# Kernel optimization log

Hardware: AMD Instinct MI355X
Metric: run time of the kernel (lower is better)

Reference implementation:

```python
import jax, jax.numpy as jnp
import numpy as np

B, S, W = 32, 128, 16
E, CD, H, P = 256, 64, 512, 256
V, CV, NC = 50000, 256, 6
CK, WK = 8, 64  # merged char/word conv kernel sizes


def conv1d(x, w, b):
    # x: [N, Cin, L], w: [Cout, Cin, K] -> [N, Cout, L-K+1] (VALID)
    y = jax.lax.conv_general_dilated(x, w, (1,), 'VALID',
                                     dimension_numbers=('NCH', 'OIH', 'NCH'))
    return y + b[None, :, None]


def setup_inputs() -> dict:
    key = jax.random.key(0)
    ks = iter(jax.random.split(key, 40))
    nrm = lambda shape: jax.random.normal(next(ks), shape, dtype=jnp.float32) * 0.05
    return {
        'seq': jax.random.randint(next(ks), (B, S), 0, V),
        'seq_char': jax.random.randint(next(ks), (B, S, W), 0, CV),
        'classes': jnp.arange(NC, dtype=jnp.int32).reshape(NC, 1),
        'embed_w': nrm((V, E)),
        'char_embed_w': nrm((CV, CD)),
        'class_embed_w': nrm((NC, E)),
        'char_conv_w': nrm((CD, CD, CK)), 'char_conv_b': nrm((CD,)),
        'word_conv_w': nrm((E, E + CD, WK)), 'word_conv_b': nrm((E,)),
        'f_Wih': nrm((4 * H, E + CD)), 'f_Whh': nrm((4 * H, H)), 'f_b': nrm((4 * H,)),
        'b_Wih': nrm((4 * H, E + CD)), 'b_Whh': nrm((4 * H, H)), 'b_b': nrm((4 * H,)),
        'attend': nrm((E, 2 * H)),
        'd_Wih': nrm((6 * H, E + 2 * H)), 'd_Whh': nrm((6 * H, 2 * H)),
        'd_bih': nrm((6 * H,)), 'd_bhh': nrm((6 * H,)),
        'proj_w': nrm((P, 2 * H)), 'proj_b': nrm((P,)),
        'cls_w': nrm((2, P)), 'cls_b': nrm((2,)),
    }


def reference(seq, seq_char, classes, embed_w, char_embed_w, class_embed_w,
              char_conv_w, char_conv_b, word_conv_w, word_conv_b,
              f_Wih, f_Whh, f_b, b_Wih, b_Whh, b_b, attend,
              d_Wih, d_Whh, d_bih, d_bhh, proj_w, proj_b, cls_w, cls_b):
    # eval-mode forward (dropout p=0.01 is identity at eval time)
    Bq, Sq = seq.shape
    pad_mask = (seq > 0).astype(jnp.float32)            # [B,S]
    word_e = jnp.tanh(embed_w[seq])                     # [B,S,E]
    # char CNN: all char convs share kernel size -> merged into one conv
    ce = char_embed_w[seq_char]                         # [B,S,W,CD]
    ce = ce.reshape(Bq * Sq, W, CD).transpose(0, 2, 1)  # [B*S, CD, W]
    char_feat = jnp.tanh(conv1d(ce, char_conv_w, char_conv_b).mean(-1).reshape(Bq, Sq, CD))
    x = jnp.concatenate([word_e, char_feat], -1)        # [B,S,E+CD]
    # word CNN over full sequence -> [B,E]
    conv_seq = jnp.tanh(conv1d(x.transpose(0, 2, 1), word_conv_w, word_conv_b).mean(-1))
    # BiLSTM; backward direction uses seq_emb[-i], i.e. order [0, S-1, ..., 1] (as in original)
    xs = x.transpose(1, 0, 2)                           # [S,B,E+CD]
    xs_b = xs[(-jnp.arange(Sq)) % Sq]

    def lstm_scan(Wih, Whh, b, inputs):
        def step(carry, xt):
            h, c = carry
            g = xt @ Wih.T + h @ Whh.T + b
            i, f, gg, o = jnp.split(g, 4, axis=-1)
            c = jax.nn.sigmoid(f) * c + jax.nn.sigmoid(i) * jnp.tanh(gg)
            h = jax.nn.sigmoid(o) * jnp.tanh(c)
            return (h, c), h
        h0 = jnp.zeros((Bq, H), x.dtype)
        _, hs = jax.lax.scan(step, (h0, h0), inputs)
        return hs

    fouts = lstm_scan(f_Wih, f_Whh, f_b, xs)            # [S,B,H]
    bouts = lstm_scan(b_Wih, b_Whh, b_b, xs_b)[::-1]    # reversed, as in original
    seq_repr = jnp.concatenate([fouts, bouts], -1)      # [S,B,2H]
    h0 = seq_repr[-1]                                   # decoder init state [B,2H]
    seq_repr = seq_repr.transpose(1, 0, 2)              # [B,S,2H]
    # class attention: the expanded attn rows are identical across positions,
    # so sum over dim 1 of the [B,S,S] bmm equals S * tanh(a_c) . seq_repr[b,t]
    a = jnp.tanh(jnp.tanh(class_embed_w[classes[:, 0]])) @ attend   # [C,2H]
    scores = Sq * jnp.einsum('ch,bth->cbt', jnp.tanh(a), seq_repr)  # [C,B,S]
    scores = scores * pad_mask[None]
    att_ctx = jnp.einsum('cbt,bth->cbh', jnp.tanh(scores), seq_repr)  # [C,B,2H]

    def gru_step(h, ctx):
        inp = jnp.concatenate([conv_seq, ctx], -1)      # [B, E+2H]
        gi = inp @ d_Wih.T + d_bih
        gh = h @ d_Whh.T + d_bhh
        ir, iz, inn = jnp.split(gi, 3, -1)
        hr, hz, hn = jnp.split(gh, 3, -1)
        r = jax.nn.sigmoid(ir + hr)
        z = jax.nn.sigmoid(iz + hz)
        n = jnp.tanh(inn + r * hn)
        h_new = jnp.tanh((1 - z) * n + z * h)           # post-tanh state fed back (as in original)
        logits = (h_new @ proj_w.T + proj_b) @ cls_w.T + cls_b
        return h_new, jax.nn.log_softmax(logits, -1)

    _, outs = jax.lax.scan(gru_step, h0, att_ctx)       # [C,B,2]
    return outs
```

## Files before the change

### kernel.cpp

```cpp
#include <hip/hip_runtime.h>

typedef __bf16 bf16_t;
typedef __bf16 bf16x8 __attribute__((ext_vector_type(8)));
typedef float f32x4 __attribute__((ext_vector_type(4)));

static constexpr int BB = 32, SS = 128, WW = 16, EE = 256, CDm = 64, HH = 512, PP = 256;
static constexpr int EC = 320;
static constexpr int H2 = 1024;
static constexpr int G6 = 3072;
static constexpr int NKT = 28;
static constexpr int NKTX = 12;

__device__ __forceinline__ float sigm(float x){ return 1.f/(1.f + expf(-x)); }

__global__ void k_embed(const int* __restrict__ seq, const float* __restrict__ embed_w,
                        float* __restrict__ x, float* __restrict__ mask){
  int bs = blockIdx.x; int c = threadIdx.x;
  int wid = seq[bs];
  x[(size_t)bs*EC + c] = tanhf(embed_w[(size_t)wid*EE + c]);
  if (c == 0) mask[bs] = (wid > 0) ? 1.f : 0.f;
}

__global__ void k_cbar(const int* __restrict__ seq_char, const float* __restrict__ cemb,
                       float* __restrict__ cbar){
  int bs = blockIdx.x; int c = threadIdx.x;
  float ce[WW];
  #pragma unroll
  for (int p = 0; p < WW; ++p){
    int id = seq_char[bs*WW + p];
    ce[p] = cemb[(size_t)id*CDm + c];
  }
  #pragma unroll
  for (int k = 0; k < 8; ++k){
    float s = 0.f;
    #pragma unroll
    for (int p = 0; p < 9; ++p) s += ce[k+p];
    cbar[(size_t)bs*512 + c*8 + k] = s * (1.f/9.f);
  }
}

__global__ __launch_bounds__(64) void k_xbar(const float* __restrict__ x, float* __restrict__ xbar){
  __shared__ float xl[64][129];
  int gid = blockIdx.x*64 + threadIdx.x;
  int b = gid / EC, c = gid % EC;
  int tl = threadIdx.x;
  for (int t = 0; t < SS; ++t) xl[tl][t] = x[((size_t)b*SS + t)*EC + c];
  float s = 0.f;
  for (int t = 0; t < 65; ++t) s += xl[tl][t];
  const float inv = 1.f/65.f;
  float* o = &xbar[(size_t)(b*EC + c)*64];
  o[0] = s*inv;
  for (int k = 1; k < 64; ++k){ s += xl[tl][k+64] - xl[tl][k-1]; o[k] = s*inv; }
}

template<int BM,int BN,int TM,int TN>
__global__ __launch_bounds__(256) void k_gemm(const float* __restrict__ A,
    const float* __restrict__ Wm, float* __restrict__ part,
    int M, int N, int K, int kslice){
  __shared__ float As[32][BM+4];
  __shared__ float Ws[32][BN+4];
  const int tid = threadIdx.x;
  const int tx = tid & 15, ty = tid >> 4;
  const int m0 = blockIdx.x*BM, n0 = blockIdx.y*BN, ks = blockIdx.z;
  const int kb = ks*kslice;
  float acc[TM][TN];
  #pragma unroll
  for (int i = 0; i < TM; ++i)
    #pragma unroll
    for (int j = 0; j < TN; ++j) acc[i][j] = 0.f;
  for (int kt = 0; kt < kslice; kt += 32){
    constexpr int AIT = (BM*8)/256;
    #pragma unroll
    for (int it = 0; it < AIT; ++it){
      int ch = tid + it*256;
      int r = ch >> 3, kc = (ch & 7)*4;
      float4 v = *(const float4*)(A + (size_t)(m0+r)*K + kb + kt + kc);
      As[kc+0][r]=v.x; As[kc+1][r]=v.y; As[kc+2][r]=v.z; As[kc+3][r]=v.w;
    }
    constexpr int WIT = (BN*8)/256;
    #pragma unroll
    for (int it = 0; it < WIT; ++it){
      int ch = tid + it*256;
      int r = ch >> 3, kc = (ch & 7)*4;
      float4 v = *(const float4*)(Wm + (size_t)(n0+r)*K + kb + kt + kc);
      Ws[kc+0][r]=v.x; Ws[kc+1][r]=v.y; Ws[kc+2][r]=v.z; Ws[kc+3][r]=v.w;
    }
    __syncthreads();
    #pragma unroll
    for (int kk = 0; kk < 32; ++kk){
      float a[TM], wv[TN];
      #pragma unroll
      for (int i = 0; i < TM; ++i) a[i] = As[kk][ty*TM+i];
      #pragma unroll
      for (int j = 0; j < TN; ++j) wv[j] = Ws[kk][tx*TN+j];
      #pragma unroll
      for (int i = 0; i < TM; ++i)
        #pragma unroll
        for (int j = 0; j < TN; ++j) acc[i][j] = fmaf(a[i], wv[j], acc[i][j]);
    }
    __syncthreads();
  }
  #pragma unroll
  for (int i = 0; i < TM; ++i){
    int row = m0 + ty*TM + i;
    #pragma unroll
    for (int j = 0; j < TN; ++j){
      int col = n0 + tx*TN + j;
      part[((size_t)ks*M + row)*N + col] = acc[i][j];
    }
  }
}

__global__ __launch_bounds__(64) void k_fin(const float* __restrict__ part,
    const float* __restrict__ bias, float* __restrict__ out,
    int M, int N, int KS, int ldc, int act){
  int col = blockIdx.x*64 + threadIdx.x;
  int row = blockIdx.y;
  float v = bias ? bias[col] : 0.f;
  for (int ks = 0; ks < KS; ++ks) v += part[((size_t)ks*M + row)*N + col];
  if (act) v = tanhf(v);
  out[(size_t)row*ldc + col] = v;
}

__global__ __launch_bounds__(64) void k_packw(const float* __restrict__ fWih, const float* __restrict__ fWhh,
    const float* __restrict__ bWih, const float* __restrict__ bWhh, bf16_t* __restrict__ Wp){
  int id = blockIdx.x;
  int kt = id % NKT; id /= NKT;
  int slice = id % 32; int dir = id / 32;
  int l = threadIdx.x;
  const float* Whh = dir ? bWhh : fWhh;
  const float* Wih = dir ? bWih : fWih;
  int krow = (l >> 4)*8;
  for (int nt = 0; nt < 4; ++nt){
    int row = nt*512 + slice*16 + (l & 15);
    bf16_t* dst = &Wp[((((size_t)(dir*32+slice)*NKT + kt)*4 + nt)*64 + l)*8];
    if (kt < 16){
      const float* src = &Whh[(size_t)row*512 + kt*32 + krow];
      #pragma unroll
      for (int r = 0; r < 8; ++r) dst[r] = (bf16_t)src[r];
    } else {
      int kx = (kt-16)*32 + krow;
      if (kx + 8 <= 320){
        const float* src = &Wih[(size_t)row*320 + kx];
        #pragma unroll
        for (int r = 0; r < 8; ++r) dst[r] = (bf16_t)src[r];
      } else {
        #pragma unroll
        for (int r = 0; r < 8; ++r) dst[r] = (bf16_t)0.f;
      }
    }
  }
}

__global__ __launch_bounds__(64) void k_packdw(const float* __restrict__ W, bf16_t* __restrict__ Wo){
  int id = blockIdx.x;
  int kt = id % 32; id /= 32;
  int nt = id % 3;  int wg = id / 3;
  int l = threadIdx.x;
  int col = nt*1024 + wg*16 + (l & 15);
  int k0 = kt*32 + (l >> 4)*8;
  bf16_t* dst = Wo + (((size_t)(wg*3 + nt)*32 + kt)*64 + l)*8;
  const float* src = W + (size_t)col*1024 + k0;
  #pragma unroll
  for (int r = 0; r < 8; ++r) dst[r] = (bf16_t)src[r];
}

__global__ __launch_bounds__(64) void k_packpw(const float* __restrict__ W, bf16_t* __restrict__ Wo){
  int id = blockIdx.x;
  int kt = id & 31, wg = id >> 5;
  int l = threadIdx.x;
  int col = wg*16 + (l & 15);
  int k0 = kt*32 + (l >> 4)*8;
  bf16_t* dst = Wo + (((size_t)wg*32 + kt)*64 + l)*8;
  const float* src = W + (size_t)col*1024 + k0;
  #pragma unroll
  for (int r = 0; r < 8; ++r) dst[r] = (bf16_t)src[r];
}

__global__ __launch_bounds__(64) void k_packx(const float* __restrict__ x, bf16_t* __restrict__ xp){
  int id = blockIdx.x;
  int ktx = id % NKTX; id /= NKTX;
  int mt = id & 1; int t = id >> 1;
  int l = threadIdx.x;
  int b = (l & 15) + 16*mt;
  int c = ktx*32 + (l >> 4)*8;
  bf16_t* dst = &xp[(((size_t)t*2 + mt)*NKTX + ktx)*64*8 + (size_t)l*8];
  if (c + 8 <= EC){
    const float* src = &x[((size_t)b*SS + t)*EC + c];
    #pragma unroll
    for (int r = 0; r < 8; ++r) dst[r] = (bf16_t)src[r];
  } else {
    #pragma unroll
    for (int r = 0; r < 8; ++r) dst[r] = (bf16_t)0.f;
  }
}

__global__ __launch_bounds__(256) void k_zero(unsigned int* __restrict__ base){
  int i = blockIdx.x*256 + threadIdx.x;
  if (i < 35840) __hip_atomic_store(base + i, 0u, __ATOMIC_RELAXED, __HIP_MEMORY_SCOPE_AGENT);
}

__global__ __launch_bounds__(64) void k_hprep(const float* __restrict__ seq_repr, bf16_t* __restrict__ hdp){
  int mt = blockIdx.x >> 5, kt = blockIdx.x & 31, l = threadIdx.x;
  int b = mt*16 + (l & 15);
  int jb = kt*32 + (l >> 4)*8;
  const float* src = &seq_repr[((size_t)b*SS + 127)*H2 + jb];
  unsigned* dst = (unsigned*)(hdp + (((size_t)mt*32 + kt)*64 + l)*8);
  #pragma unroll
  for (int p = 0; p < 4; ++p){
    unsigned pk = (unsigned)__builtin_bit_cast(unsigned short, (bf16_t)src[2*p])
                | ((unsigned)__builtin_bit_cast(unsigned short, (bf16_t)src[2*p+1]) << 16);
    __hip_atomic_store(dst + p, pk, __ATOMIC_RELAXED, __HIP_MEMORY_SCOPE_AGENT);
  }
}

__global__ __launch_bounds__(256, 1) void k_lstm(const bf16_t* __restrict__ Wp,
    const bf16_t* __restrict__ xp, bf16_t* __restrict__ hp,
    const float* __restrict__ fb, const float* __restrict__ bb,
    float* __restrict__ seq_repr, unsigned int* __restrict__ lf){
  const int wg = blockIdx.x;
  const int dir = wg >> 5, slice = wg & 31;
  const int tid = threadIdx.x;
  const int wv = tid >> 6, lane = tid & 63;
  __shared__ __align__(16) bf16_t Wl[NKT*4*64*8];
  __shared__ float red[4][32][65];
  __shared__ float bias_l[64];
  __shared__ float c_l[16][32];
  {
    const uint4* src = (const uint4*)(Wp + ((size_t)(dir*32 + slice))*NKT*4*64*8);
    uint4* dst = (uint4*)Wl;
    for (int i = tid; i < NKT*4*64*8/8; i += 256) dst[i] = src[i];
  }
  if (tid < 64){
    const float* bv = dir ? bb : fb;
    bias_l[tid] = bv[(tid >> 4)*512 + slice*16 + (tid & 15)];
  }
  ((float*)c_l)[tid]       = 0.f;
  ((float*)c_l)[tid + 256] = 0.f;
  __syncthreads();

  union HU { unsigned long long u[2]; bf16x8 v; };

  for (int t = 0; t < SS; ++t){
    const int ph = t & 1;
    const int s = dir ? ((SS - t) & 127) : t;
    f32x4 acc[2][4];
    f32x4 zero = {0.f,0.f,0.f,0.f};
    #pragma unroll
    for (int m = 0; m < 2; ++m)
      #pragma unroll
      for (int n = 0; n < 4; ++n) acc[m][n] = zero;

    const bf16_t* xb = xp + (size_t)s*2*NKTX*64*8;
    bf16x8 ax[3][2];
    #pragma unroll
    for (int i = 0; i < 3; ++i){
      int ktx = wv*3 + i;
      #pragma unroll
      for (int m = 0; m < 2; ++m)
        ax[i][m] = *reinterpret_cast<const bf16x8*>(xb + (((size_t)m*NKTX + ktx)*64 + lane)*8);
    }
    #pragma unroll
    for (int i = 0; i < 3; ++i){
      int kt = 16 + wv*3 + i;
      #pragma unroll
      for (int nt = 0; nt < 4; ++nt){
        bf16x8 Bf = *reinterpret_cast<const bf16x8*>(&Wl[(((size_t)kt*4 + nt)*64 + lane)*8]);
        acc[0][nt] = __builtin_amdgcn_mfma_f32_16x16x32_bf16(ax[i][0], Bf, acc[0][nt], 0, 0, 0);
        acc[1][nt] = __builtin_amdgcn_mfma_f32_16x16x32_bf16(ax[i][1], Bf, acc[1][nt], 0, 0, 0);
      }
    }
    if (t > 0 && lane < 8){
      int prod = dir*32 + (wv + 4*(lane >> 1))*2 + (lane & 1);
      const unsigned int* fp = lf + prod*16;
      unsigned tgt = (unsigned)t;
      for(;;){
        unsigned v = __hip_atomic_load(fp, __ATOMIC_RELAXED, __HIP_MEMORY_SCOPE_AGENT);
        if (__ballot(v < tgt) == 0ull) break;
      }
    }
    const bf16_t* hb_ = hp + ((size_t)(ph*2 + dir))*2*16*64*8;
    bf16x8 ah[4][2];
    #pragma unroll
    for (int i = 0; i < 4; ++i){
      int kt = wv + 4*i;
      #pragma unroll
      for (int m = 0; m < 2; ++m){
        const unsigned long long* p =
            (const unsigned long long*)(hb_ + (((size_t)m*16 + kt)*64 + lane)*8);
        HU u;
        u.u[0] = __hip_atomic_load(p,     __ATOMIC_RELAXED, __HIP_MEMORY_SCOPE_AGENT);
        u.u[1] = __hip_atomic_load(p + 1, __ATOMIC_RELAXED, __HIP_MEMORY_SCOPE_AGENT);
        ah[i][m] = u.v;
      }
    }
    #pragma unroll
    for (int i = 0; i < 4; ++i){
      int kt = wv + 4*i;
      #pragma unroll
      for (int nt = 0; nt < 4; ++nt){
        bf16x8 Bf = *reinterpret_cast<const bf16x8*>(&Wl[(((size_t)kt*4 + nt)*64 + lane)*8]);
        acc[0][nt] = __builtin_amdgcn_mfma_f32_16x16x32_bf16(ah[i][0], Bf, acc[0][nt], 0, 0, 0);
        acc[1][nt] = __builtin_amdgcn_mfma_f32_16x16x32_bf16(ah[i][1], Bf, acc[1][nt], 0, 0, 0);
      }
    }
    {
      int r0 = (lane >> 4)*4, cc = lane & 15;
      #pragma unroll
      for (int m = 0; m < 2; ++m)
        #pragma unroll
        for (int n = 0; n < 4; ++n)
          #pragma unroll
          for (int e = 0; e < 4; ++e)
            red[wv][m*16 + r0 + e][n*16 + cc] = acc[m][n][e];
    }
    __syncthreads();
    {
      int b = tid & 31, jjp = tid >> 5;
      float hv[2];
      #pragma unroll
      for (int u2 = 0; u2 < 2; ++u2){
        int jj = jjp*2 + u2;
        float gi_ = bias_l[jj],     gf_ = bias_l[16+jj];
        float gg_ = bias_l[32+jj],  go_ = bias_l[48+jj];
        #pragma unroll
        for (int w2 = 0; w2 < 4; ++w2){
          gi_ += red[w2][b][jj];      gf_ += red[w2][b][16+jj];
          gg_ += red[w2][b][32+jj];   go_ += red[w2][b][48+jj];
        }
        float ii = sigm(gi_), ff = sigm(gf_), g2 = tanhf(gg_), oo = sigm(go_);
        float c = ff*c_l[jj][b] + ii*g2;
        c_l[jj][b] = c;
        hv[u2] = oo*tanhf(c);
      }
      int j0 = slice*16 + jjp*2;
      int s_out = dir ? (127 - t) : t;
      float2 st; st.x = hv[0]; st.y = hv[1];
      *(float2*)&seq_repr[((size_t)b*SS + s_out)*H2 + dir*HH + j0] = st;
      int mt = b >> 4, kth = j0 >> 5, ln = (b & 15) + 16*((j0 >> 3) & 3), rg = j0 & 7;
      unsigned pk = (unsigned)__builtin_bit_cast(unsigned short, (bf16_t)hv[0])
                  | ((unsigned)__builtin_bit_cast(unsigned short, (bf16_t)hv[1]) << 16);
      unsigned* dst = (unsigned*)(hp +
          ((((size_t)((ph^1)*2 + dir)*2 + mt)*16 + kth)*64 + ln)*8 + rg);
      __hip_atomic_store(dst, pk, __ATOMIC_RELAXED, __HIP_MEMORY_SCOPE_AGENT);
    }
    __syncthreads();
    if (tid == 0)
      __hip_atomic_store(lf + wg*16, (unsigned)(t+1), __ATOMIC_RELAXED, __HIP_MEMORY_SCOPE_AGENT);
  }
}

__global__ __launch_bounds__(256) void k_ta(const int* __restrict__ classes,
    const float* __restrict__ cls_emb, const float* __restrict__ attend, float* __restrict__ ta){
  int c = blockIdx.x;
  __shared__ float t2[EE];
  int tid = threadIdx.x;
  int ci = classes[c];
  t2[tid] = tanhf(tanhf(cls_emb[(size_t)ci*EE + tid]));
  __syncthreads();
  for (int r = 0; r < 4; ++r){
    int h = r*256 + tid;
    float acc = 0.f;
    for (int e = 0; e < EE; ++e) acc = fmaf(t2[e], attend[(size_t)e*H2 + h], acc);
    ta[c*H2 + h] = tanhf(acc);
  }
}

__global__ __launch_bounds__(256) void k_ctx(const float* __restrict__ ta,
    const float* __restrict__ seq_repr, const float* __restrict__ mask, float* __restrict__ ctx){
  int c = blockIdx.x, b = blockIdx.y;
  __shared__ float ta_l[H2];
  __shared__ float ps[128][2];
  __shared__ float sc[128];
  int tid = threadIdx.x;
  for (int i = tid; i < H2; i += 256) ta_l[i] = ta[c*H2 + i];
  __syncthreads();
  {
    int tt = tid >> 1, half = tid & 1;
    const float* row = &seq_repr[((size_t)b*SS + tt)*H2 + half*512];
    const float* tl = &ta_l[half*512];
    float p = 0.f;
    for (int i = 0; i < 512; i += 4){
      float4 v = *(const float4*)&row[i];
      p = fmaf(tl[i], v.x, p);   p = fmaf(tl[i+1], v.y, p);
      p = fmaf(tl[i+2], v.z, p); p = fmaf(tl[i+3], v.w, p);
    }
    ps[tt][half] = p;
  }
  __syncthreads();
  if (tid < 128){
    float s = (ps[tid][0] + ps[tid][1]) * 128.f * mask[b*SS + tid];
    sc[tid] = tanhf(s);
  }
  __syncthreads();
  {
    int h = tid*4;
    float4 a = {0.f,0.f,0.f,0.f};
    for (int t = 0; t < SS; ++t){
      float s = sc[t];
      float4 v = *(const float4*)&seq_repr[((size_t)b*SS + t)*H2 + h];
      a.x = fmaf(s, v.x, a.x); a.y = fmaf(s, v.y, a.y);
      a.z = fmaf(s, v.z, a.z); a.w = fmaf(s, v.w, a.w);
    }
    *(float4*)&ctx[((size_t)c*BB + b)*H2 + h] = a;
  }
}

__global__ void k_inp(const float* __restrict__ conv_seq, const float* __restrict__ ctx,
                      float* __restrict__ inp){
  int cb = blockIdx.x;
  int b = cb & 31;
  for (int k = threadIdx.x; k < 1280; k += 256){
    float v = (k < 256) ? conv_seq[b*256 + k] : ctx[(size_t)cb*H2 + (k - 256)];
    inp[(size_t)cb*1280 + k] = v;
  }
}

__global__ __launch_bounds__(256, 1) void k_dec(
    const bf16_t* __restrict__ Whp, const bf16_t* __restrict__ Ppw,
    const float* __restrict__ gi, const float* __restrict__ d_bhh,
    const float* __restrict__ seq_repr,
    const float* __restrict__ proj_b, const float* __restrict__ cls_w,
    const float* __restrict__ cls_b, bf16_t* __restrict__ hdp,
    float* __restrict__ pl, unsigned int* __restrict__ dfh,
    unsigned int* __restrict__ dfpl, float* __restrict__ out){
  const int wg = blockIdx.x;
  const int tid = threadIdx.x;
  const int wv = tid >> 6, lane = tid & 63;
  __shared__ __align__(16) bf16_t Wl[3*32*64*8];
  __shared__ float red[4][32][49];
  __shared__ float plred[8][32][2];
  __shared__ float cv[2];
  {
    const uint4* src = (const uint4*)(Whp + (size_t)wg*3*32*64*8);
    uint4* dst = (uint4*)Wl;
    for (int i = tid; i < 3*32*64*8/8; i += 256) dst[i] = src[i];
  }
  const int b = tid & 31, jp = tid >> 5;
  const int j0 = wg*16 + jp*2;
  float hold[2];
  hold[0] = seq_repr[((size_t)b*SS + 127)*H2 + j0];
  hold[1] = seq_repr[((size_t)b*SS + 127)*H2 + j0 + 1];
  float bhh[3][2];
  #pragma unroll
  for (int g = 0; g < 3; ++g){
    bhh[g][0] = d_bhh[g*1024 + j0];
    bhh[g][1] = d_bhh[g*1024 + j0 + 1];
  }
  __syncthreads();
  union HU { unsigned long long u[2]; bf16x8 v; };
  const int r0 = (lane >> 4)*4, cc = lane & 15;

  for (int c = 0; c < 6; ++c){
    if (c > 0){
      const unsigned int* fp = dfh + lane*16;
      unsigned tgt = (unsigned)c;
      for(;;){
        unsigned v = __hip_atomic_load(fp, __ATOMIC_RELAXED, __HIP_MEMORY_SCOPE_AGENT);
        if (__ballot(v < tgt) == 0ull) break;
      }
    }
    f32x4 acc[2][3];
    f32x4 zero = {0.f,0.f,0.f,0.f};
    #pragma unroll
    for (int m = 0; m < 2; ++m)
      #pragma unroll
      for (int n = 0; n < 3; ++n) acc[m][n] = zero;
    const bf16_t* hb = hdp + (size_t)(c & 1)*2*32*64*8;
    #pragma unroll
    for (int i = 0; i < 8; ++i){
      int kt = wv*8 + i;
      HU u0, u1;
      const unsigned long long* p0 = (const unsigned long long*)(hb + (((size_t)0*32 + kt)*64 + lane)*8);
      const unsigned long long* p1 = (const unsigned long long*)(hb + (((size_t)1*32 + kt)*64 + lane)*8);
      u0.u[0] = __hip_atomic_load(p0,     __ATOMIC_RELAXED, __HIP_MEMORY_SCOPE_AGENT);
      u0.u[1] = __hip_atomic_load(p0 + 1, __ATOMIC_RELAXED, __HIP_MEMORY_SCOPE_AGENT);
      u1.u[0] = __hip_atomic_load(p1,     __ATOMIC_RELAXED, __HIP_MEMORY_SCOPE_AGENT);
      u1.u[1] = __hip_atomic_load(p1 + 1, __ATOMIC_RELAXED, __HIP_MEMORY_SCOPE_AGENT);
      #pragma unroll
      for (int nt = 0; nt < 3; ++nt){
        bf16x8 Bf = *reinterpret_cast<const bf16x8*>(&Wl[(((size_t)nt*32 + kt)*64 + lane)*8]);
        acc[0][nt] = __builtin_amdgcn_mfma_f32_16x16x32_bf16(u0.v, Bf, acc[0][nt], 0, 0, 0);
        acc[1][nt] = __builtin_amdgcn_mfma_f32_16x16x32_bf16(u1.v, Bf, acc[1][nt], 0, 0, 0);
      }
    }
    #pragma unroll
    for (int m = 0; m < 2; ++m)
      #pragma unroll
      for (int n = 0; n < 3; ++n)
        #pragma unroll
        for (int e = 0; e < 4; ++e)
          red[wv][m*16 + r0 + e][n*16 + cc] = acc[m][n][e];
    __syncthreads();
    float hnew[2];
    #pragma unroll
    for (int u2 = 0; u2 < 2; ++u2){
      int jj = jp*2 + u2;
      float r_ = 0.f, z_ = 0.f, n_ = 0.f;
      #pragma unroll
      for (int w = 0; w < 4; ++w){
        r_ += red[w][b][jj]; z_ += red[w][b][16+jj]; n_ += red[w][b][32+jj];
      }
      const float* gr = gi + ((size_t)(c*BB) + b)*G6 + wg*16 + jj;
      float rr = sigm(gr[0]    + bhh[0][u2] + r_);
      float zz = sigm(gr[1024] + bhh[1][u2] + z_);
      float nn = tanhf(gr[2048] + rr*(bhh[2][u2] + n_));
      hnew[u2] = tanhf((1.f - zz)*nn + zz*hold[u2]);
      hold[u2] = hnew[u2];
    }
    {
      int kt = j0 >> 5, ln = (b & 15) + 16*((j0 >> 3) & 3), rg = j0 & 7, mt = b >> 4;
      unsigned pk = (unsigned)__builtin_bit_cast(unsigned short, (bf16_t)hnew[0])
                  | ((unsigned)__builtin_bit_cast(unsigned short, (bf16_t)hnew[1]) << 16);
      unsigned* dst = (unsigned*)(hdp + (size_t)((c+1)&1)*2*32*64*8 +
                                  (((size_t)(mt*32 + kt)*64 + ln)*8 + rg));
      __hip_atomic_store(dst, pk, __ATOMIC_RELAXED, __HIP_MEMORY_SCOPE_AGENT);
    }
    __syncthreads();
    if (tid == 0)
      __hip_atomic_store(dfh + wg*16, (unsigned)(c+1), __ATOMIC_RELAXED, __HIP_MEMORY_SCOPE_AGENT);
    if (wg < 16){
      {
        const unsigned int* fp = dfh + lane*16;
        unsigned tgt = (unsigned)(c+1);
        for(;;){
          unsigned v = __hip_atomic_load(fp, __ATOMIC_RELAXED, __HIP_MEMORY_SCOPE_AGENT);
          if (__ballot(v < tgt) == 0ull) break;
        }
      }
      f32x4 pacc[2] = {zero, zero};
      const bf16_t* hb2 = hdp + (size_t)((c+1)&1)*2*32*64*8;
      #pragma unroll
      for (int i = 0; i < 8; ++i){
        int kt = wv*8 + i;
        HU u0, u1;
        const unsigned long long* p0 = (const unsigned long long*)(hb2 + (((size_t)0*32 + kt)*64 + lane)*8);
        const unsigned long long* p1 = (const unsigned long long*)(hb2 + (((size_t)1*32 + kt)*64 + lane)*8);
        u0.u[0] = __hip_atomic_load(p0,     __ATOMIC_RELAXED, __HIP_MEMORY_SCOPE_AGENT);
        u0.u[1] = __hip_atomic_load(p0 + 1, __ATOMIC_RELAXED, __HIP_MEMORY_SCOPE_AGENT);
        u1.u[0] = __hip_atomic_load(p1,     __ATOMIC_RELAXED, __HIP_MEMORY_SCOPE_AGENT);
        u1.u[1] = __hip_atomic_load(p1 + 1, __ATOMIC_RELAXED, __HIP_MEMORY_SCOPE_AGENT);
        bf16x8 Bf = *reinterpret_cast<const bf16x8*>(Ppw + (((size_t)wg*32 + kt)*64 + lane)*8);
        pacc[0] = __builtin_amdgcn_mfma_f32_16x16x32_bf16(u0.v, Bf, pacc[0], 0, 0, 0);
        pacc[1] = __builtin_amdgcn_mfma_f32_16x16x32_bf16(u1.v, Bf, pacc[1], 0, 0, 0);
      }
      #pragma unroll
      for (int m = 0; m < 2; ++m)
        #pragma unroll
        for (int e = 0; e < 4; ++e)
          red[wv][m*16 + r0 + e][cc] = pacc[m][e];
      __syncthreads();
      {
        int colp = tid >> 5;
        float v0 = 0.f, v1 = 0.f;
        #pragma unroll
        for (int w = 0; w < 4; ++w){
          v0 += red[w][b][colp*2];
          v1 += red[w][b][colp*2+1];
        }
        int c0 = wg*16 + colp*2, c1 = c0 + 1;
        plred[colp][b][0] = v0*cls_w[c0]      + v1*cls_w[c1];
        plred[colp][b][1] = v0*cls_w[PP + c0] + v1*cls_w[PP + c1];
      }
      __syncthreads();
      if (tid < 32){
        float s0 = 0.f, s1 = 0.f;
        #pragma unroll
        for (int g = 0; g < 8; ++g){ s0 += plred[g][tid][0]; s1 += plred[g][tid][1]; }
        unsigned* dp = (unsigned*)(pl + (((size_t)c*16 + wg)*32 + tid)*2);
        __hip_atomic_store(dp,     __builtin_bit_cast(unsigned, s0), __ATOMIC_RELAXED, __HIP_MEMORY_SCOPE_AGENT);
        __hip_atomic_store(dp + 1, __builtin_bit_cast(unsigned, s1), __ATOMIC_RELAXED, __HIP_MEMORY_SCOPE_AGENT);
      }
      __syncthreads();
      if (tid == 0)
        __hip_atomic_store(dfpl + wg*16, (unsigned)(c+1), __ATOMIC_RELAXED, __HIP_MEMORY_SCOPE_AGENT);
    }
  }
  if (wg == 0){
    if (lane < 16){
      const unsigned int* fp = dfpl + lane*16;
      for(;;){
        unsigned v = __hip_atomic_load(fp, __ATOMIC_RELAXED, __HIP_MEMORY_SCOPE_AGENT);
        if (__ballot(v < 6u) == 0ull) break;
      }
    }
    __syncthreads();
    float* cr = (float*)red;
    cr[tid*2]   = proj_b[tid]*cls_w[tid];
    cr[tid*2+1] = proj_b[tid]*cls_w[PP + tid];
    __syncthreads();
    if (tid < 2){
      float s = 0.f;
      for (int i = 0; i < 256; ++i) s += cr[i*2 + tid];
      cv[tid] = s;
    }
    __syncthreads();
    if (tid < 32){
      for (int c = 0; c < 6; ++c){
        float a0 = cv[0] + cls_b[0], a1 = cv[1] + cls_b[1];
        for (int w = 0; w < 16; ++w){
          const unsigned* dp = (const unsigned*)(pl + (((size_t)c*16 + w)*32 + tid)*2);
          a0 += __builtin_bit_cast(float, __hip_atomic_load(dp,     __ATOMIC_RELAXED, __HIP_MEMORY_SCOPE_AGENT));
          a1 += __builtin_bit_cast(float, __hip_atomic_load(dp + 1, __ATOMIC_RELAXED, __HIP_MEMORY_SCOPE_AGENT));
        }
        float mx = fmaxf(a0, a1);
        float ls = mx + logf(expf(a0 - mx) + expf(a1 - mx));
        out[((size_t)c*BB + tid)*2 + 0] = a0 - ls;
        out[((size_t)c*BB + tid)*2 + 1] = a1 - ls;
      }
    }
  }
}

extern "C" void kernel_launch(void* const* d_in, const int* in_sizes, int n_in,
                              void* d_out, int out_size, void* d_ws, size_t ws_size,
                              hipStream_t stream){
  const int*   seq          = (const int*)  d_in[0];
  const int*   seq_char     = (const int*)  d_in[1];
  const int*   classes      = (const int*)  d_in[2];
  const float* embed_w      = (const float*)d_in[3];
  const float* char_embed_w = (const float*)d_in[4];
  const float* class_embed_w= (const float*)d_in[5];
  const float* char_conv_w  = (const float*)d_in[6];
  const float* char_conv_b  = (const float*)d_in[7];
  const float* word_conv_w  = (const float*)d_in[8];
  const float* word_conv_b  = (const float*)d_in[9];
  const float* f_Wih = (const float*)d_in[10];
  const float* f_Whh = (const float*)d_in[11];
  const float* f_b   = (const float*)d_in[12];
  const float* b_Wih = (const float*)d_in[13];
  const float* b_Whh = (const float*)d_in[14];
  const float* b_b   = (const float*)d_in[15];
  const float* attend = (const float*)d_in[16];
  const float* d_Wih  = (const float*)d_in[17];
  const float* d_Whh  = (const float*)d_in[18];
  const float* d_bih  = (const float*)d_in[19];
  const float* d_bhh  = (const float*)d_in[20];
  const float* proj_w = (const float*)d_in[21];
  const float* proj_b = (const float*)d_in[22];
  const float* cls_w  = (const float*)d_in[23];
  const float* cls_b  = (const float*)d_in[24];
  float* out = (float*)d_out;

  char* wsb = (char*)d_ws;
  size_t off = 0;
  auto alloc = [&](size_t bytes) -> char* {
    char* p = wsb + off;
    off += (bytes + 255) & ~(size_t)255;
    return p;
  };
  unsigned int* flags = (unsigned int*)alloc(12288);
  unsigned int* lf   = flags;
  unsigned int* dfh  = flags + 1024;
  unsigned int* dfpl = flags + 2048;
  bf16_t* hp  = (bf16_t*)alloc((size_t)2*2*2*16*64*8 * 2);
  bf16_t* hdp = (bf16_t*)alloc((size_t)2*2*32*64*8 * 2);
  bf16_t* Wp  = (bf16_t*)alloc((size_t)2*32*NKT*4*64*8 * 2);
  bf16_t* Whp = (bf16_t*)alloc((size_t)64*3*32*64*8 * 2);
  bf16_t* Ppw = (bf16_t*)alloc((size_t)16*32*64*8 * 2);
  bf16_t* xp  = (bf16_t*)alloc((size_t)128*2*NKTX*64*8 * 2);
  float* pl       = (float*)alloc((size_t)6*16*32*2*4);
  float* x        = (float*)alloc((size_t)BB*SS*EC*4);
  float* mask     = (float*)alloc((size_t)BB*SS*4);
  float* cbar     = (float*)alloc((size_t)4096*512*4);
  float* xbar     = (float*)alloc((size_t)BB*EC*64*4);
  float* conv_seq = (float*)alloc((size_t)BB*256*4);
  float* seq_repr = (float*)alloc((size_t)BB*SS*H2*4);
  float* ta       = (float*)alloc((size_t)6*H2*4);
  float* ctx      = (float*)alloc((size_t)6*BB*H2*4);
  float* inp      = (float*)alloc((size_t)192*1280*4);
  float* gi       = (float*)alloc((size_t)192*G6*4);
  float* part_char= (float*)alloc((size_t)2*4096*64*4);
  float* part_word= (float*)alloc((size_t)32*BB*256*4);
  float* part_gi  = (float*)alloc((size_t)4*192*G6*4);
  (void)ws_size; (void)in_sizes; (void)n_in; (void)out_size;

  k_zero<<<140, 256, 0, stream>>>((unsigned int*)d_ws);

  k_packw<<<2*32*NKT, 64, 0, stream>>>(f_Wih, f_Whh, b_Wih, b_Whh, Wp);
  k_packdw<<<64*3*32, 64, 0, stream>>>(d_Whh, Whp);
  k_packpw<<<16*32, 64, 0, stream>>>(proj_w, Ppw);
  k_embed<<<BB*SS, 256, 0, stream>>>(seq, embed_w, x, mask);
  k_cbar<<<BB*SS, 64, 0, stream>>>(seq_char, char_embed_w, cbar);
  k_gemm<32,64,2,4><<<dim3(128,1,2), 256, 0, stream>>>(cbar, char_conv_w, part_char, 4096, 64, 512, 256);
  k_fin<<<dim3(1,4096), 64, 0, stream>>>(part_char, char_conv_b, x + 256, 4096, 64, 2, EC, 1);
  k_xbar<<<160, 64, 0, stream>>>(x, xbar);
  k_gemm<32,64,2,4><<<dim3(1,4,32), 256, 0, stream>>>(xbar, word_conv_w, part_word, 32, 256, 20480, 640);
  k_fin<<<dim3(4,32), 64, 0, stream>>>(part_word, word_conv_b, conv_seq, 32, 256, 32, 256, 1);
  k_packx<<<128*2*NKTX, 64, 0, stream>>>(x, xp);
  k_lstm<<<64, 256, 0, stream>>>(Wp, xp, hp, f_b, b_b, seq_repr, lf);
  k_ta<<<6, 256, 0, stream>>>(classes, class_embed_w, attend, ta);
  k_ctx<<<dim3(6,32), 256, 0, stream>>>(ta, seq_repr, mask, ctx);
  k_inp<<<192, 256, 0, stream>>>(conv_seq, ctx, inp);
  k_gemm<64,64,4,4><<<dim3(3,48,4), 256, 0, stream>>>(inp, d_Wih, part_gi, 192, G6, 1280, 320);
  k_fin<<<dim3(48,192), 64, 0, stream>>>(part_gi, d_bih, gi, 192, G6, 4, G6, 0);
  k_hprep<<<64, 64, 0, stream>>>(seq_repr, hdp);
  k_dec<<<64, 256, 0, stream>>>(Whp, Ppw, gi, d_bhh, seq_repr, proj_b, cls_w, cls_b,
                                hdp, pl, dfh, dfpl, out);
}
```

Measured before the change: 663.7 us.

## Replace per-step flag barriers with step-tagged hidden-state words in LSTM and GRU

Each bf16 hidden value now carries a 16-bit step tag in its own 32-bit word. Consumers in the LSTM and decoder kernels spin on the data itself until every tag matches the expected step. This removes the separate flag store/poll round trip and the trailing workgroup barrier before publishing a flag. In exchange the hidden-state buffers double in size, more bytes are polled per step, and the zeroed workspace region grows.

Result: slower. 879.7 us (+32.5%).

```diff
diff --git a/kernel.cpp b/kernel.cpp
--- a/kernel.cpp
+++ b/kernel.cpp
@@ -3,6 +3,8 @@
 typedef __bf16 bf16_t;
 typedef __bf16 bf16x8 __attribute__((ext_vector_type(8)));
 typedef float f32x4 __attribute__((ext_vector_type(4)));
+typedef unsigned u32x4 __attribute__((ext_vector_type(4)));
+typedef unsigned long long u64;
 
 static constexpr int BB = 32, SS = 128, WW = 16, EE = 256, CDm = 64, HH = 512, PP = 256;
 static constexpr int EC = 320;
@@ -12,6 +14,9 @@
 static constexpr int NKTX = 12;
 
 __device__ __forceinline__ float sigm(float x){ return 1.f/(1.f + expf(-x)); }
+
+#define ALOAD(p)    __hip_atomic_load((p),  __ATOMIC_RELAXED, __HIP_MEMORY_SCOPE_AGENT)
+#define ASTORE(p,v) __hip_atomic_store((p),(v),__ATOMIC_RELAXED, __HIP_MEMORY_SCOPE_AGENT)
 
 __global__ void k_embed(const int* __restrict__ seq, const float* __restrict__ embed_w,
                         float* __restrict__ x, float* __restrict__ mask){
@@ -195,29 +200,30 @@
   }
 }
 
-__global__ __launch_bounds__(256) void k_zero(unsigned int* __restrict__ base){
+__global__ __launch_bounds__(256) void k_zero(unsigned int* __restrict__ base, int n){
   int i = blockIdx.x*256 + threadIdx.x;
-  if (i < 35840) __hip_atomic_store(base + i, 0u, __ATOMIC_RELAXED, __HIP_MEMORY_SCOPE_AGENT);
-}
-
-__global__ __launch_bounds__(64) void k_hprep(const float* __restrict__ seq_repr, bf16_t* __restrict__ hdp){
+  if (i < n) ASTORE(base + i, 0u);
+}
+
+__global__ __launch_bounds__(64) void k_hprep(const float* __restrict__ seq_repr,
+                                              unsigned* __restrict__ hdp){
   int mt = blockIdx.x >> 5, kt = blockIdx.x & 31, l = threadIdx.x;
   int b = mt*16 + (l & 15);
   int jb = kt*32 + (l >> 4)*8;
   const float* src = &seq_repr[((size_t)b*SS + 127)*H2 + jb];
-  unsigned* dst = (unsigned*)(hdp + (((size_t)mt*32 + kt)*64 + l)*8);
+  u64* dst = (u64*)(hdp + (((size_t)mt*32 + kt)*64 + l)*8);
   #pragma unroll
   for (int p = 0; p < 4; ++p){
-    unsigned pk = (unsigned)__builtin_bit_cast(unsigned short, (bf16_t)src[2*p])
-                | ((unsigned)__builtin_bit_cast(unsigned short, (bf16_t)src[2*p+1]) << 16);
-    __hip_atomic_store(dst + p, pk, __ATOMIC_RELAXED, __HIP_MEMORY_SCOPE_AGENT);
+    u64 lo = (u64)(unsigned)__builtin_bit_cast(unsigned short, (bf16_t)src[2*p]);
+    u64 hi = (u64)(unsigned)__builtin_bit_cast(unsigned short, (bf16_t)src[2*p+1]);
+    ASTORE(dst + p, lo | (hi << 32));
   }
 }
 
 __global__ __launch_bounds__(256, 1) void k_lstm(const bf16_t* __restrict__ Wp,
-    const bf16_t* __restrict__ xp, bf16_t* __restrict__ hp,
+    const bf16_t* __restrict__ xp, unsigned* __restrict__ thp,
     const float* __restrict__ fb, const float* __restrict__ bb,
-    float* __restrict__ seq_repr, unsigned int* __restrict__ lf){
+    float* __restrict__ seq_repr){
   const int wg = blockIdx.x;
   const int dir = wg >> 5, slice = wg & 31;
   const int tid = threadIdx.x;
@@ -239,7 +245,7 @@
   ((float*)c_l)[tid + 256] = 0.f;
   __syncthreads();
 
-  union HU { unsigned long long u[2]; bf16x8 v; };
+  const u64* hq = (const u64*)thp;
 
   for (int t = 0; t < SS; ++t){
     const int ph = t & 1;
@@ -260,6 +266,17 @@
       for (int m = 0; m < 2; ++m)
         ax[i][m] = *reinterpret_cast<const bf16x8*>(xb + (((size_t)m*NKTX + ktx)*64 + lane)*8);
     }
+    u64 raw[4][2][4];
+    #pragma unroll
+    for (int i = 0; i < 4; ++i){
+      int kt = wv + 4*i;
+      #pragma unroll
+      for (int m = 0; m < 2; ++m){
+        const u64* p = hq + ((((size_t)(ph*2 + dir)*2 + m)*16 + kt)*64 + lane)*4;
+        #pragma unroll
+        for (int q = 0; q < 4; ++q) raw[i][m][q] = ALOAD(p + q);
+      }
+    }
     #pragma unroll
     for (int i = 0; i < 3; ++i){
       int kt = 16 + wv*3 + i;
@@ -270,38 +287,47 @@
         acc[1][nt] = __builtin_amdgcn_mfma_f32_16x16x32_bf16(ax[i][1], Bf, acc[1][nt], 0, 0, 0);
       }
     }
-    if (t > 0 && lane < 8){
-      int prod = dir*32 + (wv + 4*(lane >> 1))*2 + (lane & 1);
-      const unsigned int* fp = lf + prod*16;
-      unsigned tgt = (unsigned)t;
-      for(;;){
-        unsigned v = __hip_atomic_load(fp, __ATOMIC_RELAXED, __HIP_MEMORY_SCOPE_AGENT);
-        if (__ballot(v < tgt) == 0ull) break;
-      }
-    }
-    const bf16_t* hb_ = hp + ((size_t)(ph*2 + dir))*2*16*64*8;
-    bf16x8 ah[4][2];
+    const u64 tagpat = (u64)t * 0x0000000100000001ull;
+    for (;;){
+      bool ok = true;
+      #pragma unroll
+      for (int i = 0; i < 4; ++i)
+        #pragma unroll
+        for (int m = 0; m < 2; ++m)
+          #pragma unroll
+          for (int q = 0; q < 4; ++q)
+            ok &= (((raw[i][m][q] >> 16) & 0x0000FFFF0000FFFFull) == tagpat);
+      if (__ballot(!ok) == 0ull) break;
+      __builtin_amdgcn_s_sleep(1);
+      #pragma unroll
+      for (int i = 0; i < 4; ++i){
+        int kt = wv + 4*i;
+        #pragma unroll
+        for (int m = 0; m < 2; ++m){
+          const u64* p = hq + ((((size_t)(ph*2 + dir)*2 + m)*16 + kt)*64 + lane)*4;
+          #pragma unroll
+          for (int q = 0; q < 4; ++q) raw[i][m][q] = ALOAD(p + q);
+        }
+      }
+    }
     #pragma unroll
     for (int i = 0; i < 4; ++i){
       int kt = wv + 4*i;
+      bf16x8 a[2];
       #pragma unroll
       for (int m = 0; m < 2; ++m){
-        const unsigned long long* p =
-            (const unsigned long long*)(hb_ + (((size_t)m*16 + kt)*64 + lane)*8);
-        HU u;
-        u.u[0] = __hip_atomic_load(p,     __ATOMIC_RELAXED, __HIP_MEMORY_SCOPE_AGENT);
-        u.u[1] = __hip_atomic_load(p + 1, __ATOMIC_RELAXED, __HIP_MEMORY_SCOPE_AGENT);
-        ah[i][m] = u.v;
-      }
-    }
-    #pragma unroll
-    for (int i = 0; i < 4; ++i){
-      int kt = wv + 4*i;
+        u32x4 w;
+        #pragma unroll
+        for (int q = 0; q < 4; ++q)
+          w[q] = __builtin_amdgcn_perm((unsigned)(raw[i][m][q] >> 32),
+                                       (unsigned)raw[i][m][q], 0x05040100u);
+        a[m] = __builtin_bit_cast(bf16x8, w);
+      }
       #pragma unroll
       for (int nt = 0; nt < 4; ++nt){
         bf16x8 Bf = *reinterpret_cast<const bf16x8*>(&Wl[(((size_t)kt*4 + nt)*64 + lane)*8]);
-        acc[0][nt] = __builtin_amdgcn_mfma_f32_16x16x32_bf16(ah[i][0], Bf, acc[0][nt], 0, 0, 0);
-        acc[1][nt] = __builtin_amdgcn_mfma_f32_16x16x32_bf16(ah[i][1], Bf, acc[1][nt], 0, 0, 0);
+        acc[0][nt] = __builtin_amdgcn_mfma_f32_16x16x32_bf16(a[0], Bf, acc[0][nt], 0, 0, 0);
+        acc[1][nt] = __builtin_amdgcn_mfma_f32_16x16x32_bf16(a[1], Bf, acc[1][nt], 0, 0, 0);
       }
     }
     {
@@ -337,16 +363,14 @@
       int s_out = dir ? (127 - t) : t;
       float2 st; st.x = hv[0]; st.y = hv[1];
       *(float2*)&seq_repr[((size_t)b*SS + s_out)*H2 + dir*HH + j0] = st;
-      int mt = b >> 4, kth = j0 >> 5, ln = (b & 15) + 16*((j0 >> 3) & 3), rg = j0 & 7;
-      unsigned pk = (unsigned)__builtin_bit_cast(unsigned short, (bf16_t)hv[0])
-                  | ((unsigned)__builtin_bit_cast(unsigned short, (bf16_t)hv[1]) << 16);
-      unsigned* dst = (unsigned*)(hp +
-          ((((size_t)((ph^1)*2 + dir)*2 + mt)*16 + kth)*64 + ln)*8 + rg);
-      __hip_atomic_store(dst, pk, __ATOMIC_RELAXED, __HIP_MEMORY_SCOPE_AGENT);
-    }
-    __syncthreads();
-    if (tid == 0)
-      __hip_atomic_store(lf + wg*16, (unsigned)(t+1), __ATOMIC_RELAXED, __HIP_MEMORY_SCOPE_AGENT);
+      int mt = b >> 4, kth = j0 >> 5, ln = (b & 15) + 16*((j0 >> 3) & 3);
+      unsigned tg = (unsigned)(t+1) << 16;
+      u64 lo = (u64)((unsigned)__builtin_bit_cast(unsigned short, (bf16_t)hv[0]) | tg);
+      u64 hi = (u64)((unsigned)__builtin_bit_cast(unsigned short, (bf16_t)hv[1]) | tg);
+      u64* dst = (u64*)thp + ((((size_t)((ph^1)*2 + dir)*2 + mt)*16 + kth)*64 + ln)*4 + ((j0 & 7) >> 1);
+      ASTORE(dst, lo | (hi << 32));
+    }
+    __syncthreads();
   }
 }
 
@@ -421,9 +445,8 @@
     const float* __restrict__ gi, const float* __restrict__ d_bhh,
     const float* __restrict__ seq_repr,
     const float* __restrict__ proj_b, const float* __restrict__ cls_w,
-    const float* __restrict__ cls_b, bf16_t* __restrict__ hdp,
-    float* __restrict__ pl, unsigned int* __restrict__ dfh,
-    unsigned int* __restrict__ dfpl, float* __restrict__ out){
+    const float* __restrict__ cls_b, unsigned* __restrict__ hdp,
+    float* __restrict__ pl, unsigned int* __restrict__ dfpl, float* __restrict__ out){
   const int wg = blockIdx.x;
   const int tid = threadIdx.x;
   const int wv = tid >> 6, lane = tid & 63;
@@ -448,40 +471,63 @@
     bhh[g][1] = d_bhh[g*1024 + j0 + 1];
   }
   __syncthreads();
-  union HU { unsigned long long u[2]; bf16x8 v; };
+  const u64* hq = (const u64*)hdp;
   const int r0 = (lane >> 4)*4, cc = lane & 15;
 
   for (int c = 0; c < 6; ++c){
-    if (c > 0){
-      const unsigned int* fp = dfh + lane*16;
-      unsigned tgt = (unsigned)c;
-      for(;;){
-        unsigned v = __hip_atomic_load(fp, __ATOMIC_RELAXED, __HIP_MEMORY_SCOPE_AGENT);
-        if (__ballot(v < tgt) == 0ull) break;
-      }
-    }
     f32x4 acc[2][3];
     f32x4 zero = {0.f,0.f,0.f,0.f};
     #pragma unroll
     for (int m = 0; m < 2; ++m)
       #pragma unroll
       for (int n = 0; n < 3; ++n) acc[m][n] = zero;
-    const bf16_t* hb = hdp + (size_t)(c & 1)*2*32*64*8;
-    #pragma unroll
-    for (int i = 0; i < 8; ++i){
-      int kt = wv*8 + i;
-      HU u0, u1;
-      const unsigned long long* p0 = (const unsigned long long*)(hb + (((size_t)0*32 + kt)*64 + lane)*8);
-      const unsigned long long* p1 = (const unsigned long long*)(hb + (((size_t)1*32 + kt)*64 + lane)*8);
-      u0.u[0] = __hip_atomic_load(p0,     __ATOMIC_RELAXED, __HIP_MEMORY_SCOPE_AGENT);
-      u0.u[1] = __hip_atomic_load(p0 + 1, __ATOMIC_RELAXED, __HIP_MEMORY_SCOPE_AGENT);
-      u1.u[0] = __hip_atomic_load(p1,     __ATOMIC_RELAXED, __HIP_MEMORY_SCOPE_AGENT);
-      u1.u[1] = __hip_atomic_load(p1 + 1, __ATOMIC_RELAXED, __HIP_MEMORY_SCOPE_AGENT);
-      #pragma unroll
-      for (int nt = 0; nt < 3; ++nt){
-        bf16x8 Bf = *reinterpret_cast<const bf16x8*>(&Wl[(((size_t)nt*32 + kt)*64 + lane)*8]);
-        acc[0][nt] = __builtin_amdgcn_mfma_f32_16x16x32_bf16(u0.v, Bf, acc[0][nt], 0, 0, 0);
-        acc[1][nt] = __builtin_amdgcn_mfma_f32_16x16x32_bf16(u1.v, Bf, acc[1][nt], 0, 0, 0);
+    const u64 tagpat = (u64)c * 0x0000000100000001ull;
+    #pragma unroll
+    for (int g = 0; g < 2; ++g){
+      u64 raw[4][2][4];
+      bool first = true;
+      for (;;){
+        if (!first) __builtin_amdgcn_s_sleep(1);
+        first = false;
+        #pragma unroll
+        for (int i = 0; i < 4; ++i){
+          int kt = wv*8 + g*4 + i;
+          #pragma unroll
+          for (int m = 0; m < 2; ++m){
+            const u64* p = hq + ((((size_t)(c & 1)*2 + m)*32 + kt)*64 + lane)*4;
+            #pragma unroll
+            for (int q = 0; q < 4; ++q) raw[i][m][q] = ALOAD(p + q);
+          }
+        }
+        bool ok = true;
+        #pragma unroll
+        for (int i = 0; i < 4; ++i)
+          #pragma unroll
+          for (int m = 0; m < 2; ++m)
+            #pragma unroll
+            for (int q = 0; q < 4; ++q)
+              ok &= (((raw[i][m][q] >> 16) & 0x0000FFFF0000FFFFull) == tagpat);
+        if (__ballot(!ok) == 0ull) break;
+      }
+      #pragma unroll
+      for (int i = 0; i < 4; ++i){
+        int kt = wv*8 + g*4 + i;
+        bf16x8 a[2];
+        #pragma unroll
+        for (int m = 0; m < 2; ++m){
+          u32x4 w;
+          #pragma unroll
+          for (int q = 0; q < 4; ++q)
+            w[q] = __builtin_amdgcn_perm((unsigned)(raw[i][m][q] >> 32),
+                                         (unsigned)raw[i][m][q], 0x05040100u);
+          a[m] = __builtin_bit_cast(bf16x8, w);
+        }
+        #pragma unroll
+        for (int nt = 0; nt < 3; ++nt){
+          bf16x8 Bf = *reinterpret_cast<const bf16x8*>(&Wl[(((size_t)nt*32 + kt)*64 + lane)*8]);
+          acc[0][nt] = __builtin_amdgcn_mfma_f32_16x16x32_bf16(a[0], Bf, acc[0][nt], 0, 0, 0);
+          acc[1][nt] = __builtin_amdgcn_mfma_f32_16x16x32_bf16(a[1], Bf, acc[1][nt], 0, 0, 0);
+        }
       }
     }
     #pragma unroll
@@ -509,40 +555,61 @@
       hold[u2] = hnew[u2];
     }
     {
-      int kt = j0 >> 5, ln = (b & 15) + 16*((j0 >> 3) & 3), rg = j0 & 7, mt = b >> 4;
-      unsigned pk = (unsigned)__builtin_bit_cast(unsigned short, (bf16_t)hnew[0])
-                  | ((unsigned)__builtin_bit_cast(unsigned short, (bf16_t)hnew[1]) << 16);
-      unsigned* dst = (unsigned*)(hdp + (size_t)((c+1)&1)*2*32*64*8 +
-                                  (((size_t)(mt*32 + kt)*64 + ln)*8 + rg));
-      __hip_atomic_store(dst, pk, __ATOMIC_RELAXED, __HIP_MEMORY_SCOPE_AGENT);
-    }
-    __syncthreads();
-    if (tid == 0)
-      __hip_atomic_store(dfh + wg*16, (unsigned)(c+1), __ATOMIC_RELAXED, __HIP_MEMORY_SCOPE_AGENT);
+      int kt = j0 >> 5, ln = (b & 15) + 16*((j0 >> 3) & 3), mt = b >> 4;
+      unsigned tg = (unsigned)(c+1) << 16;
+      u64 lo = (u64)((unsigned)__builtin_bit_cast(unsigned short, (bf16_t)hnew[0]) | tg);
+      u64 hi = (u64)((unsigned)__builtin_bit_cast(unsigned short, (bf16_t)hnew[1]) | tg);
+      u64* dst = (u64*)hdp + ((((size_t)((c+1) & 1)*2 + mt)*32 + kt)*64 + ln)*4 + ((j0 & 7) >> 1);
+      ASTORE(dst, lo | (hi << 32));
+    }
+    __syncthreads();
     if (wg < 16){
-      {
-        const unsigned int* fp = dfh + lane*16;
-        unsigned tgt = (unsigned)(c+1);
-        for(;;){
-          unsigned v = __hip_atomic_load(fp, __ATOMIC_RELAXED, __HIP_MEMORY_SCOPE_AGENT);
-          if (__ballot(v < tgt) == 0ull) break;
-        }
-      }
+      const u64 tagp2 = (u64)(c+1) * 0x0000000100000001ull;
       f32x4 pacc[2] = {zero, zero};
-      const bf16_t* hb2 = hdp + (size_t)((c+1)&1)*2*32*64*8;
-      #pragma unroll
-      for (int i = 0; i < 8; ++i){
-        int kt = wv*8 + i;
-        HU u0, u1;
-        const unsigned long long* p0 = (const unsigned long long*)(hb2 + (((size_t)0*32 + kt)*64 + lane)*8);
-        const unsigned long long* p1 = (const unsigned long long*)(hb2 + (((size_t)1*32 + kt)*64 + lane)*8);
-        u0.u[0] = __hip_atomic_load(p0,     __ATOMIC_RELAXED, __HIP_MEMORY_SCOPE_AGENT);
-        u0.u[1] = __hip_atomic_load(p0 + 1, __ATOMIC_RELAXED, __HIP_MEMORY_SCOPE_AGENT);
-        u1.u[0] = __hip_atomic_load(p1,     __ATOMIC_RELAXED, __HIP_MEMORY_SCOPE_AGENT);
-        u1.u[1] = __hip_atomic_load(p1 + 1, __ATOMIC_RELAXED, __HIP_MEMORY_SCOPE_AGENT);
-        bf16x8 Bf = *reinterpret_cast<const bf16x8*>(Ppw + (((size_t)wg*32 + kt)*64 + lane)*8);
-        pacc[0] = __builtin_amdgcn_mfma_f32_16x16x32_bf16(u0.v, Bf, pacc[0], 0, 0, 0);
-        pacc[1] = __builtin_amdgcn_mfma_f32_16x16x32_bf16(u1.v, Bf, pacc[1], 0, 0, 0);
+      #pragma unroll
+      for (int g = 0; g < 2; ++g){
+        u64 raw[4][2][4];
+        bool first = true;
+        for (;;){
+          if (!first) __builtin_amdgcn_s_sleep(1);
+          first = false;
+          #pragma unroll
+          for (int i = 0; i < 4; ++i){
+            int kt = wv*8 + g*4 + i;
+            #pragma unroll
+            for (int m = 0; m < 2; ++m){
+              const u64* p = hq + ((((size_t)((c+1) & 1)*2 + m)*32 + kt)*64 + lane)*4;
+              #pragma unroll
+              for (int q = 0; q < 4; ++q) raw[i][m][q] = ALOAD(p + q);
+            }
+          }
+          bool ok = true;
+          #pragma unroll
+          for (int i = 0; i < 4; ++i)
+            #pragma unroll
+            for (int m = 0; m < 2; ++m)
+              #pragma unroll
+              for (int q = 0; q < 4; ++q)
+                ok &= (((raw[i][m][q] >> 16) & 0x0000FFFF0000FFFFull) == tagp2);
+          if (__ballot(!ok) == 0ull) break;
+        }
+        #pragma unroll
+        for (int i = 0; i < 4; ++i){
+          int kt = wv*8 + g*4 + i;
+          bf16x8 a[2];
+          #pragma unroll
+          for (int m = 0; m < 2; ++m){
+            u32x4 w;
+            #pragma unroll
+            for (int q = 0; q < 4; ++q)
+              w[q] = __builtin_amdgcn_perm((unsigned)(raw[i][m][q] >> 32),
+                                           (unsigned)raw[i][m][q], 0x05040100u);
+            a[m] = __builtin_bit_cast(bf16x8, w);
+          }
+          bf16x8 Bf = *reinterpret_cast<const bf16x8*>(Ppw + (((size_t)wg*32 + kt)*64 + lane)*8);
+          pacc[0] = __builtin_amdgcn_mfma_f32_16x16x32_bf16(a[0], Bf, pacc[0], 0, 0, 0);
+          pacc[1] = __builtin_amdgcn_mfma_f32_16x16x32_bf16(a[1], Bf, pacc[1], 0, 0, 0);
+        }
       }
       #pragma unroll
       for (int m = 0; m < 2; ++m)
@@ -568,19 +635,19 @@
         #pragma unroll
         for (int g = 0; g < 8; ++g){ s0 += plred[g][tid][0]; s1 += plred[g][tid][1]; }
         unsigned* dp = (unsigned*)(pl + (((size_t)c*16 + wg)*32 + tid)*2);
-        __hip_atomic_store(dp,     __builtin_bit_cast(unsigned, s0), __ATOMIC_RELAXED, __HIP_MEMORY_SCOPE_AGENT);
-        __hip_atomic_store(dp + 1, __builtin_bit_cast(unsigned, s1), __ATOMIC_RELAXED, __HIP_MEMORY_SCOPE_AGENT);
+        ASTORE(dp,     __builtin_bit_cast(unsigned, s0));
+        ASTORE(dp + 1, __builtin_bit_cast(unsigned, s1));
       }
       __syncthreads();
       if (tid == 0)
-        __hip_atomic_store(dfpl + wg*16, (unsigned)(c+1), __ATOMIC_RELAXED, __HIP_MEMORY_SCOPE_AGENT);
+        ASTORE(dfpl + wg*16, (unsigned)(c+1));
     }
   }
   if (wg == 0){
     if (lane < 16){
       const unsigned int* fp = dfpl + lane*16;
       for(;;){
-        unsigned v = __hip_atomic_load(fp, __ATOMIC_RELAXED, __HIP_MEMORY_SCOPE_AGENT);
+        unsigned v = ALOAD(fp);
         if (__ballot(v < 6u) == 0ull) break;
       }
     }
@@ -600,8 +667,8 @@
         float a0 = cv[0] + cls_b[0], a1 = cv[1] + cls_b[1];
         for (int w = 0; w < 16; ++w){
           const unsigned* dp = (const unsigned*)(pl + (((size_t)c*16 + w)*32 + tid)*2);
-          a0 += __builtin_bit_cast(float, __hip_atomic_load(dp,     __ATOMIC_RELAXED, __HIP_MEMORY_SCOPE_AGENT));
-          a1 += __builtin_bit_cast(float, __hip_atomic_load(dp + 1, __ATOMIC_RELAXED, __HIP_MEMORY_SCOPE_AGENT));
+          a0 += __builtin_bit_cast(float, ALOAD(dp));
+          a1 += __builtin_bit_cast(float, ALOAD(dp + 1));
         }
         float mx = fmaxf(a0, a1);
         float ls = mx + logf(expf(a0 - mx) + expf(a1 - mx));
@@ -650,11 +717,10 @@
     return p;
   };
   unsigned int* flags = (unsigned int*)alloc(12288);
-  unsigned int* lf   = flags;
-  unsigned int* dfh  = flags + 1024;
   unsigned int* dfpl = flags + 2048;
-  bf16_t* hp  = (bf16_t*)alloc((size_t)2*2*2*16*64*8 * 2);
-  bf16_t* hdp = (bf16_t*)alloc((size_t)2*2*32*64*8 * 2);
+  unsigned* thp = (unsigned*)alloc((size_t)2*2*2*16*64*8 * 4);
+  unsigned* hdp = (unsigned*)alloc((size_t)2*2*32*64*8 * 4);
+  const int ZERO_DWORDS = 3072 + 65536 + 65536;
   bf16_t* Wp  = (bf16_t*)alloc((size_t)2*32*NKT*4*64*8 * 2);
   bf16_t* Whp = (bf16_t*)alloc((size_t)64*3*32*64*8 * 2);
   bf16_t* Ppw = (bf16_t*)alloc((size_t)16*32*64*8 * 2);
@@ -675,7 +741,7 @@
   float* part_gi  = (float*)alloc((size_t)4*192*G6*4);
   (void)ws_size; (void)in_sizes; (void)n_in; (void)out_size;
 
-  k_zero<<<140, 256, 0, stream>>>((unsigned int*)d_ws);
+  k_zero<<<(ZERO_DWORDS + 255)/256, 256, 0, stream>>>((unsigned int*)d_ws, ZERO_DWORDS);
 
   k_packw<<<2*32*NKT, 64, 0, stream>>>(f_Wih, f_Whh, b_Wih, b_Whh, Wp);
   k_packdw<<<64*3*32, 64, 0, stream>>>(d_Whh, Whp);
@@ -688,7 +754,7 @@
   k_gemm<32,64,2,4><<<dim3(1,4,32), 256, 0, stream>>>(xbar, word_conv_w, part_word, 32, 256, 20480, 640);
   k_fin<<<dim3(4,32), 64, 0, stream>>>(part_word, word_conv_b, conv_seq, 32, 256, 32, 256, 1);
   k_packx<<<128*2*NKTX, 64, 0, stream>>>(x, xp);
-  k_lstm<<<64, 256, 0, stream>>>(Wp, xp, hp, f_b, b_b, seq_repr, lf);
+  k_lstm<<<64, 256, 0, stream>>>(Wp, xp, thp, f_b, b_b, seq_repr);
   k_ta<<<6, 256, 0, stream>>>(classes, class_embed_w, attend, ta);
   k_ctx<<<dim3(6,32), 256, 0, stream>>>(ta, seq_repr, mask, ctx);
   k_inp<<<192, 256, 0, stream>>>(conv_seq, ctx, inp);
@@ -696,5 +762,5 @@
   k_fin<<<dim3(48,192), 64, 0, stream>>>(part_gi, d_bih, gi, 192, G6, 4, G6, 0);
   k_hprep<<<64, 64, 0, stream>>>(seq_repr, hdp);
   k_dec<<<64, 256, 0, stream>>>(Whp, Ppw, gi, d_bhh, seq_repr, proj_b, cls_w, cls_b,
-                                hdp, pl, dfh, dfpl, out);
-}
+                                hdp, pl, dfpl, out);
+}
```
